# Optimization experiments

Measured on AMD Instinct MI355X. Metric: run time of the kernel, lower is better.

## Reference

```python
import jax, jax.numpy as jnp
import numpy as np

CUTOFF = 5.0
N_ENV = 8
F0, F1 = 16, 32  # filter_dims
D = 256          # feature_dim


def setup_inputs() -> dict:
    key = jax.random.key(0)
    ks = jax.random.split(key, 12)
    B, E, N = 128, 64, 32
    r = jax.random.normal(ks[0], (B, E, 3), jnp.float32) * 3.0
    # neighbors placed near r so distances fall inside the cutoff
    r_nb = r[..., None, :] + jax.random.normal(ks[1], (B, E, N, 3), jnp.float32) * 1.5
    ee_scales = jax.random.uniform(ks[2], (N_ENV,), jnp.float32, 0.5, CUTOFF)
    ee_kernel = jax.random.normal(ks[3], (4, F0), jnp.float32) / jnp.sqrt(4.0)
    ee_bias = jax.random.normal(ks[4], (F0,), jnp.float32) * 2.0
    beta_kernel = jax.random.normal(ks[5], (F0 + N_ENV, F1), jnp.float32) / jnp.sqrt(F0 + N_ENV + 0.0)
    beta_bias = jnp.zeros((F1,), jnp.float32)
    gamma_kernel = jax.random.normal(ks[6], (F1, D), jnp.float32) / jnp.sqrt(F1 + 0.0)
    dense1_kernel = jax.random.normal(ks[7], (4, D), jnp.float32) / jnp.sqrt(4.0)
    dense1_bias = jnp.zeros((D,), jnp.float32)
    out_kernel = jax.random.normal(ks[8], (D, D), jnp.float32) / jnp.sqrt(D + 0.0)
    out_bias = jnp.zeros((D,), jnp.float32)
    return dict(r=r, r_nb=r_nb, ee_scales=ee_scales, ee_kernel=ee_kernel, ee_bias=ee_bias,
                beta_kernel=beta_kernel, beta_bias=beta_bias, gamma_kernel=gamma_kernel,
                dense1_kernel=dense1_kernel, dense1_bias=dense1_bias,
                out_kernel=out_kernel, out_bias=out_bias)


def reference(r, r_nb, ee_scales, ee_kernel, ee_bias, beta_kernel, beta_bias,
              gamma_kernel, dense1_kernel, dense1_bias, out_kernel, out_bias):
    # pairwise diff features: [dist, dx, dy, dz] per neighbor
    diff = r_nb - r[..., None, :]                       # [B,E,N,3]
    dist = jnp.linalg.norm(diff, axis=-1, keepdims=True)  # [B,E,N,1]
    feats = jnp.concatenate([dist, diff], axis=-1)      # [B,E,N,4]

    # PairwiseFilter (beta_ee): envelopes + small dense, gated by smooth cutoff
    env = jnp.exp(-jnp.square(dist / ee_scales))        # [B,E,N,N_ENV]
    h = jnp.tanh(feats @ ee_kernel + ee_bias)           # [B,E,N,F0]
    x = dist / CUTOFF
    fcut = jnp.where(x < 1.0, 0.5 * (jnp.cos(jnp.pi * x) + 1.0), 0.0)
    beta = (jnp.concatenate([h, env], axis=-1) @ beta_kernel + beta_bias) * fcut  # [B,E,N,F1]

    gamma = beta @ gamma_kernel                         # [B,E,N,D]

    # rescale features: first column (dist) becomes log1p(dist)
    inp = feats / dist * jnp.log1p(dist)                # [B,E,N,4]
    feat = jax.nn.silu(inp @ dense1_kernel + dense1_bias)  # [B,E,N,D]

    res = jnp.einsum('...id,...id->...d', feat, gamma)  # sum over neighbors -> [B,E,D]
    res = jax.nn.silu(res @ out_kernel + out_bias)
    return res
```

## Files before the change

### kernel.cpp

```cpp
#include <hip/hip_runtime.h>
#include <hip/hip_bf16.h>

constexpr int NB   = 32;
constexpr int NENV = 8;
constexpr int F0   = 16;
constexpr int F1   = 32;
constexpr int D    = 256;
constexpr int PAIRS = 128 * 64;
constexpr float CUT = 5.0f;
constexpr int WT_STRIDE = 264;

typedef float f32x4 __attribute__((ext_vector_type(4)));
typedef short s16x8 __attribute__((ext_vector_type(8)));

__device__ __forceinline__ float fast_rcp(float x) { return __builtin_amdgcn_rcpf(x); }
__device__ __forceinline__ float silu(float a) {
  return a * fast_rcp(1.0f + __expf(-a));
}
__device__ __forceinline__ float fast_tanh(float t) {
  return 1.0f - 2.0f * fast_rcp(__expf(2.0f * t) + 1.0f);
}
__device__ __forceinline__ unsigned short f2bf(float f) {
  __hip_bfloat16 h = __float2bfloat16(f);
  unsigned short u; __builtin_memcpy(&u, &h, 2); return u;
}

__global__ __launch_bounds__(256)
__attribute__((amdgpu_waves_per_eu(4, 4)))
void moon_phase12(
    const float* __restrict__ r,
    const float* __restrict__ r_nb,
    const float* __restrict__ ee_scales,
    const float* __restrict__ ee_kernel,
    const float* __restrict__ ee_bias,
    const float* __restrict__ beta_kernel,
    const float* __restrict__ beta_bias,
    const float* __restrict__ gamma_kernel,
    const float* __restrict__ dense1_kernel,
    const float* __restrict__ dense1_bias,
    const float* __restrict__ out_kernel,
    unsigned short* __restrict__ resh,
    unsigned short* __restrict__ wt)
{
  __shared__ float s_eek[4 * F0];
  __shared__ float s_eeb[F0];
  __shared__ float s_bk[(F0 + NENV) * F1];
  __shared__ float s_bb[F1];
  __shared__ float s_is2[NENV];
  __shared__ unsigned short s_ghT[4][D * 8];
  __shared__ unsigned short s_d1kT[D * 8];
  __shared__ unsigned short s_betah[4][4][NB * 8];
  __shared__ unsigned short s_inph[4][NB * 8];
  __shared__ float s_res[4][D];

  const int tid = threadIdx.x;
  const int w   = tid >> 6;
  const int l   = tid & 63;
  const int be  = blockIdx.x * 4 + w;

  if (blockIdx.x < 64) {
    const int i  = blockIdx.x * 256 + tid;
    const int d  = i >> 6;
    const int kg = i & 63;
    ushort4 p;
    p.x = f2bf(out_kernel[(4 * kg + 0) * D + d]);
    p.y = f2bf(out_kernel[(4 * kg + 1) * D + d]);
    p.z = f2bf(out_kernel[(4 * kg + 2) * D + d]);
    p.w = f2bf(out_kernel[(4 * kg + 3) * D + d]);
    *(ushort4*)&wt[d * WT_STRIDE + 4 * kg] = p;
  }

  for (int i = tid; i < 888; i += 256) {
    if (i < 64)        s_eek[i]       = ee_kernel[i];
    else if (i < 80)   s_eeb[i - 64]  = ee_bias[i - 64];
    else if (i < 848)  s_bk[i - 80]   = beta_kernel[i - 80];
    else if (i < 880)  s_bb[i - 848]  = beta_bias[i - 848];
    else { float s = ee_scales[i - 880]; s_is2[i - 880] = 1.0f / (s * s); }
  }
  {
    const int d = tid;
    unsigned int pk[16];
    #pragma unroll
    for (int k2 = 0; k2 < 16; ++k2) {
      unsigned short lo = f2bf(gamma_kernel[(2 * k2 + 0) * D + d]);
      unsigned short hi = f2bf(gamma_kernel[(2 * k2 + 1) * D + d]);
      pk[k2] = (unsigned int)lo | ((unsigned int)hi << 16);
    }
    #pragma unroll
    for (int g = 0; g < 4; ++g)
      *(uint4*)&s_ghT[g][d * 8] = make_uint4(pk[4*g], pk[4*g+1], pk[4*g+2], pk[4*g+3]);
  }
  {
    const int d = tid;
    unsigned int p0 = (unsigned int)f2bf(0.25f * dense1_kernel[0 * D + d])
                    | ((unsigned int)f2bf(0.25f * dense1_kernel[1 * D + d]) << 16);
    unsigned int p1 = (unsigned int)f2bf(0.25f * dense1_kernel[2 * D + d])
                    | ((unsigned int)f2bf(0.25f * dense1_kernel[3 * D + d]) << 16);
    unsigned int p2 = (unsigned int)f2bf(0.25f * dense1_bias[d]);
    *(uint4*)&s_d1kT[d * 8] = make_uint4(p0, p1, p2, 0u);
  }

  __syncthreads();

  {
    const int n  = l & 31;
    const int cg = l >> 5;
    float rx = r[be * 3 + 0];
    float ry = r[be * 3 + 1];
    float rz = r[be * 3 + 2];
    const float* rn = r_nb + (be * NB + n) * 3;
    float dx = rn[0] - rx;
    float dy = rn[1] - ry;
    float dz = rn[2] - rz;
    float d2 = dx * dx + dy * dy + dz * dz;
    float dist = sqrtf(d2);
    float feats[4] = {dist, dx, dy, dz};
    float h[F0];
    #pragma unroll
    for (int j = 0; j < F0; ++j) {
      float t = s_eeb[j];
      #pragma unroll
      for (int i = 0; i < 4; ++i) t += feats[i] * s_eek[i * F0 + j];
      h[j] = fast_tanh(t);
    }
    float env[NENV];
    #pragma unroll
    for (int s = 0; s < NENV; ++s) env[s] = __expf(-d2 * s_is2[s]);
    float xc = dist * (1.0f / CUT);
    float fcut = (xc < 1.0f)
               ? 0.5f * (__cosf(3.14159265358979323846f * xc) + 1.0f)
               : 0.0f;
    if (cg == 0) {
      float lp = log1pf(dist);
      float inv = lp / dist;
      unsigned int q0 = (unsigned int)f2bf(lp) | ((unsigned int)f2bf(dx * inv) << 16);
      unsigned int q1 = (unsigned int)f2bf(dy * inv) | ((unsigned int)f2bf(dz * inv) << 16);
      *(uint4*)&s_inph[w][n * 8] = make_uint4(q0, q1, 0x3F80u , 0u);
    }
    unsigned int pk[8];
    #pragma unroll
    for (int c4 = 0; c4 < 4; ++c4) {
      float bb[4];
      #pragma unroll
      for (int cc = 0; cc < 4; ++cc) {
        int c = cg * 16 + c4 * 4 + cc;
        float a = s_bb[c];
        #pragma unroll
        for (int k = 0; k < F0; ++k) a += h[k] * s_bk[k * F1 + c];
        #pragma unroll
        for (int s = 0; s < NENV; ++s) a += env[s] * s_bk[(F0 + s) * F1 + c];
        bb[cc] = a * fcut;
      }
      pk[c4 * 2 + 0] = (unsigned int)f2bf(bb[0]) | ((unsigned int)f2bf(bb[1]) << 16);
      pk[c4 * 2 + 1] = (unsigned int)f2bf(bb[2]) | ((unsigned int)f2bf(bb[3]) << 16);
    }
    *(uint4*)&s_betah[w][2 * cg + 0][n * 8] = make_uint4(pk[0], pk[1], pk[2], pk[3]);
    *(uint4*)&s_betah[w][2 * cg + 1][n * 8] = make_uint4(pk[4], pk[5], pk[6], pk[7]);
  }
  __syncthreads();

  const int li = l & 15;
  const int g  = l >> 4;

  s16x8 a0 = *(const s16x8*)&s_betah[w][g][(0 * 16 + li) * 8];
  s16x8 a1 = *(const s16x8*)&s_betah[w][g][(1 * 16 + li) * 8];
  s16x8 ai0 = *(const s16x8*)&s_inph[w][(0 * 16 + li) * 8];
  s16x8 ai1 = *(const s16x8*)&s_inph[w][(1 * 16 + li) * 8];

  #pragma unroll 4
  for (int nt = 0; nt < 16; ++nt) {
    const int d = nt * 16 + li;
    s16x8 b  = *(const s16x8*)&s_ghT[g][d * 8];
    s16x8 bd = *(const s16x8*)&s_d1kT[d * 8];
    f32x4 z = {0.f, 0.f, 0.f, 0.f};
    f32x4 c0 = __builtin_amdgcn_mfma_f32_16x16x32_bf16(a0, b, z, 0, 0, 0);
    f32x4 c1 = __builtin_amdgcn_mfma_f32_16x16x32_bf16(a1, b, z, 0, 0, 0);
    f32x4 f0 = __builtin_amdgcn_mfma_f32_16x16x32_bf16(ai0, bd, z, 0, 0, 0);
    f32x4 f1 = __builtin_amdgcn_mfma_f32_16x16x32_bf16(ai1, bd, z, 0, 0, 0);
    float p = 0.f;
    #pragma unroll
    for (int reg = 0; reg < 4; ++reg) {
      p += silu(f0[reg]) * c0[reg];
      p += silu(f1[reg]) * c1[reg];
    }
    p += __shfl_xor(p, 16);
    p += __shfl_xor(p, 32);
    if (g == (nt & 3)) s_res[w][nt * 16 + li] = p;
  }
  float4 rv = *(const float4*)&s_res[w][4 * l];
  ushort4 rp;
  rp.x = f2bf(rv.x); rp.y = f2bf(rv.y); rp.z = f2bf(rv.z); rp.w = f2bf(rv.w);
  *(ushort4*)(resh + be * D + 4 * l) = rp;
}

__global__ __launch_bounds__(256, 4) void moon_outgemm(
    const unsigned short* __restrict__ resh,
    const unsigned short* __restrict__ wt,
    const float* __restrict__ bias,
    float* __restrict__ out)
{
  const int tid  = threadIdx.x;
  const int w    = tid >> 6;
  const int l    = tid & 63;
  const int li   = l & 15;
  const int g    = l >> 4;
  const int tile = blockIdx.x >> 1;
  const int half = blockIdx.x & 1;
  const int row0 = tile * 16;
  const int col0 = half * 128 + w * 32;

  float bi[2];
  #pragma unroll
  for (int nt = 0; nt < 2; ++nt) bi[nt] = bias[col0 + nt * 16 + li];

  f32x4 acc[2] = {{0.f,0.f,0.f,0.f},{0.f,0.f,0.f,0.f}};
  const unsigned short* ap = resh + (row0 + li) * D + g * 8;
  const unsigned short* bp = wt + (col0 + li) * WT_STRIDE + g * 8;

  #pragma unroll
  for (int ks = 0; ks < 8; ++ks) {
    s16x8 a = *(const s16x8*)(ap + ks * 32);
    #pragma unroll
    for (int nt = 0; nt < 2; ++nt) {
      s16x8 b = *(const s16x8*)(bp + nt * 16 * WT_STRIDE + ks * 32);
      acc[nt] = __builtin_amdgcn_mfma_f32_16x16x32_bf16(a, b, acc[nt], 0, 0, 0);
    }
  }
  #pragma unroll
  for (int nt = 0; nt < 2; ++nt) {
    #pragma unroll
    for (int reg = 0; reg < 4; ++reg) {
      int row = row0 + g * 4 + reg;
      int col = col0 + nt * 16 + li;
      out[row * D + col] = silu(acc[nt][reg] + bi[nt]);
    }
  }
}

extern "C" void kernel_launch(void* const* d_in, const int* in_sizes, int n_in,
                              void* d_out, int out_size, void* d_ws, size_t ws_size,
                              hipStream_t stream) {
  const float* r            = (const float*)d_in[0];
  const float* r_nb         = (const float*)d_in[1];
  const float* ee_scales    = (const float*)d_in[2];
  const float* ee_kernel    = (const float*)d_in[3];
  const float* ee_bias      = (const float*)d_in[4];
  const float* beta_kernel  = (const float*)d_in[5];
  const float* beta_bias    = (const float*)d_in[6];
  const float* gamma_kernel = (const float*)d_in[7];
  const float* dense1_kernel= (const float*)d_in[8];
  const float* dense1_bias  = (const float*)d_in[9];
  const float* out_kernel   = (const float*)d_in[10];
  const float* out_bias     = (const float*)d_in[11];
  float* out = (float*)d_out;

  unsigned short* resh = (unsigned short*)d_ws;
  unsigned short* wt   = (unsigned short*)((char*)d_ws + 4 * 1024 * 1024);

  hipLaunchKernelGGL(moon_phase12, dim3(PAIRS / 4), dim3(256), 0, stream,
                     r, r_nb, ee_scales, ee_kernel, ee_bias,
                     beta_kernel, beta_bias, gamma_kernel,
                     dense1_kernel, dense1_bias, out_kernel, resh, wt);
  hipLaunchKernelGGL(moon_outgemm, dim3(PAIRS / 16 * 2), dim3(256), 0, stream,
                     resh, wt, out_bias, out);
}
```

Measured before the change: 124.6 us.

## Fuse output GEMM into main kernel and split weight prep into own launch

The final res @ out_kernel GEMM plus SiLU now runs inside the main per-pair kernel. It reads the block's four result rows from shared memory, so the intermediate bf16 buffer is never written to or read back from global memory. The bf16 transpose of out_kernel moves into a small separate prep kernel that runs first, which fixes the earlier dependence on blocks of the same launch having finished writing it. In exchange, each block uses a 16-row MFMA tile while only 4 rows are valid, so three quarters of that GEMM's work is wasted. Every block also re-reads the full weight matrix from global memory or cache.

```diff
diff --git a/kernel.cpp b/kernel.cpp
--- a/kernel.cpp
+++ b/kernel.cpp
@@ -25,9 +25,24 @@
   unsigned short u; __builtin_memcpy(&u, &h, 2); return u;
 }
 
+__global__ __launch_bounds__(256) void moon_prep(
+    const float* __restrict__ out_kernel,
+    unsigned short* __restrict__ wt)
+{
+  const int i  = blockIdx.x * 256 + threadIdx.x;
+  const int d  = i >> 6;
+  const int kg = i & 63;
+  ushort4 p;
+  p.x = f2bf(out_kernel[(4 * kg + 0) * D + d]);
+  p.y = f2bf(out_kernel[(4 * kg + 1) * D + d]);
+  p.z = f2bf(out_kernel[(4 * kg + 2) * D + d]);
+  p.w = f2bf(out_kernel[(4 * kg + 3) * D + d]);
+  *(ushort4*)&wt[d * WT_STRIDE + 4 * kg] = p;
+}
+
 __global__ __launch_bounds__(256)
 __attribute__((amdgpu_waves_per_eu(4, 4)))
-void moon_phase12(
+void moon_fused(
     const float* __restrict__ r,
     const float* __restrict__ r_nb,
     const float* __restrict__ ee_scales,
@@ -38,9 +53,9 @@
     const float* __restrict__ gamma_kernel,
     const float* __restrict__ dense1_kernel,
     const float* __restrict__ dense1_bias,
-    const float* __restrict__ out_kernel,
-    unsigned short* __restrict__ resh,
-    unsigned short* __restrict__ wt)
+    const unsigned short* __restrict__ wt,
+    const float* __restrict__ out_bias,
+    float* __restrict__ out)
 {
   __shared__ float s_eek[4 * F0];
   __shared__ float s_eeb[F0];
@@ -51,24 +66,13 @@
   __shared__ unsigned short s_d1kT[D * 8];
   __shared__ unsigned short s_betah[4][4][NB * 8];
   __shared__ unsigned short s_inph[4][NB * 8];
-  __shared__ float s_res[4][D];
+  __shared__ unsigned short s_resall[4 * 264];
 
   const int tid = threadIdx.x;
   const int w   = tid >> 6;
   const int l   = tid & 63;
   const int be  = blockIdx.x * 4 + w;
-
-  if (blockIdx.x < 64) {
-    const int i  = blockIdx.x * 256 + tid;
-    const int d  = i >> 6;
-    const int kg = i & 63;
-    ushort4 p;
-    p.x = f2bf(out_kernel[(4 * kg + 0) * D + d]);
-    p.y = f2bf(out_kernel[(4 * kg + 1) * D + d]);
-    p.z = f2bf(out_kernel[(4 * kg + 2) * D + d]);
-    p.w = f2bf(out_kernel[(4 * kg + 3) * D + d]);
-    *(ushort4*)&wt[d * WT_STRIDE + 4 * kg] = p;
-  }
+  const int be0 = blockIdx.x * 4;
 
   for (int i = tid; i < 888; i += 256) {
     if (i < 64)        s_eek[i]       = ee_kernel[i];
@@ -185,54 +189,37 @@
     }
     p += __shfl_xor(p, 16);
     p += __shfl_xor(p, 32);
-    if (g == (nt & 3)) s_res[w][nt * 16 + li] = p;
-  }
-  float4 rv = *(const float4*)&s_res[w][4 * l];
-  ushort4 rp;
-  rp.x = f2bf(rv.x); rp.y = f2bf(rv.y); rp.z = f2bf(rv.z); rp.w = f2bf(rv.w);
-  *(ushort4*)(resh + be * D + 4 * l) = rp;
-}
-
-__global__ __launch_bounds__(256, 4) void moon_outgemm(
-    const unsigned short* __restrict__ resh,
-    const unsigned short* __restrict__ wt,
-    const float* __restrict__ bias,
-    float* __restrict__ out)
-{
-  const int tid  = threadIdx.x;
-  const int w    = tid >> 6;
-  const int l    = tid & 63;
-  const int li   = l & 15;
-  const int g    = l >> 4;
-  const int tile = blockIdx.x >> 1;
-  const int half = blockIdx.x & 1;
-  const int row0 = tile * 16;
-  const int col0 = half * 128 + w * 32;
-
-  float bi[2];
-  #pragma unroll
-  for (int nt = 0; nt < 2; ++nt) bi[nt] = bias[col0 + nt * 16 + li];
-
-  f32x4 acc[2] = {{0.f,0.f,0.f,0.f},{0.f,0.f,0.f,0.f}};
-  const unsigned short* ap = resh + (row0 + li) * D + g * 8;
-  const unsigned short* bp = wt + (col0 + li) * WT_STRIDE + g * 8;
-
-  #pragma unroll
-  for (int ks = 0; ks < 8; ++ks) {
-    s16x8 a = *(const s16x8*)(ap + ks * 32);
-    #pragma unroll
-    for (int nt = 0; nt < 2; ++nt) {
-      s16x8 b = *(const s16x8*)(bp + nt * 16 * WT_STRIDE + ks * 32);
-      acc[nt] = __builtin_amdgcn_mfma_f32_16x16x32_bf16(a, b, acc[nt], 0, 0, 0);
-    }
-  }
-  #pragma unroll
-  for (int nt = 0; nt < 2; ++nt) {
-    #pragma unroll
-    for (int reg = 0; reg < 4; ++reg) {
-      int row = row0 + g * 4 + reg;
-      int col = col0 + nt * 16 + li;
-      out[row * D + col] = silu(acc[nt][reg] + bi[nt]);
+    if (g == (nt & 3)) s_resall[w * 264 + nt * 16 + li] = f2bf(p);
+  }
+  __syncthreads();
+
+  {
+    const int col0 = w * 64;
+    float bi[4];
+    #pragma unroll
+    for (int nt = 0; nt < 4; ++nt) bi[nt] = out_bias[col0 + nt * 16 + li];
+
+    f32x4 acc[4] = {{0.f,0.f,0.f,0.f},{0.f,0.f,0.f,0.f},{0.f,0.f,0.f,0.f},{0.f,0.f,0.f,0.f}};
+    const unsigned short* arow = &s_resall[(li & 3) * 264 + g * 8];
+    const unsigned short* bp   = wt + (col0 + li) * WT_STRIDE + g * 8;
+
+    #pragma unroll
+    for (int ks = 0; ks < 8; ++ks) {
+      s16x8 a = *(const s16x8*)(arow + ks * 32);
+      #pragma unroll
+      for (int nt = 0; nt < 4; ++nt) {
+        s16x8 b = *(const s16x8*)(bp + nt * 16 * WT_STRIDE + ks * 32);
+        acc[nt] = __builtin_amdgcn_mfma_f32_16x16x32_bf16(a, b, acc[nt], 0, 0, 0);
+      }
+    }
+    if (g == 0) {
+      #pragma unroll
+      for (int nt = 0; nt < 4; ++nt) {
+        #pragma unroll
+        for (int reg = 0; reg < 4; ++reg) {
+          out[(be0 + reg) * D + col0 + nt * 16 + li] = silu(acc[nt][reg] + bi[nt]);
+        }
+      }
     }
   }
 }
@@ -254,13 +241,11 @@
   const float* out_bias     = (const float*)d_in[11];
   float* out = (float*)d_out;
 
-  unsigned short* resh = (unsigned short*)d_ws;
-  unsigned short* wt   = (unsigned short*)((char*)d_ws + 4 * 1024 * 1024);
-
-  hipLaunchKernelGGL(moon_phase12, dim3(PAIRS / 4), dim3(256), 0, stream,
+  unsigned short* wt = (unsigned short*)d_ws;
+
+  hipLaunchKernelGGL(moon_prep, dim3(64), dim3(256), 0, stream, out_kernel, wt);
+  hipLaunchKernelGGL(moon_fused, dim3(PAIRS / 4), dim3(256), 0, stream,
                      r, r_nb, ee_scales, ee_kernel, ee_bias,
                      beta_kernel, beta_bias, gamma_kernel,
-                     dense1_kernel, dense1_bias, out_kernel, resh, wt);
-  hipLaunchKernelGGL(moon_outgemm, dim3(PAIRS / 16 * 2), dim3(256), 0, stream,
-                     resh, wt, out_bias, out);
-}
+                     dense1_kernel, dense1_bias, wt, out_bias, out);
+}
```

New measurement: 124.2 us. Within noise of the previous version (-0.3%).
